# Kernel optimization log

Measured on AMD Instinct MI355X. Metric: run time of the kernel, lower is better.

## Reference

```python
import jax, jax.numpy as jnp
import numpy as np

# ---- config (matches init_kwargs) ----
B, NP, DIM, HEADS, DH, NDIM = 32, 576, 512, 8, 64, 16
N = NP + 1                 # seq len incl cls token = 577
INNER = HEADS * DH         # 512


def setup_inputs() -> dict:
    key = jax.random.key(0)
    ks = jax.random.split(key, 11)
    D2 = 2 * DIM  # bidirectional EMA doubles kernel dim
    return {
        "x": jax.random.normal(ks[0], (B, N, DIM), jnp.float32),
        "W_qk": jax.random.normal(ks[1], (DIM, 2 * INNER), jnp.float32) / np.float32(np.sqrt(DIM)),
        "W_v": jax.random.normal(ks[2], (DIM, INNER), jnp.float32) / np.float32(np.sqrt(DIM)),
        "W_out": jax.random.normal(ks[3], (INNER, DIM), jnp.float32) / np.float32(np.sqrt(INNER)),
        "b_out": jnp.zeros((DIM,), jnp.float32),
        "rel_bias": jax.random.normal(ks[4], (2 * N - 1,), jnp.float32) * 0.02,
        "ema_delta": jax.random.normal(ks[5], (D2, NDIM, 1), jnp.float32),
        "ema_alpha": jax.random.normal(ks[6], (D2, NDIM, 1), jnp.float32),
        "ema_beta": jax.random.normal(ks[7], (D2, NDIM, 1), jnp.float32) * 0.5,
        "ema_gamma": jax.random.normal(ks[8], (D2, NDIM), jnp.float32) * 0.5,
        "ema_omega": jax.random.normal(ks[9], (DIM,), jnp.float32),
    }


def _ema_move(x, delta, alpha, beta, gamma, omega):
    """Bidirectional MultiHeadEMA (MEGA) via FFT convolution. x: (B, L, D)."""
    b, L, d = x.shape
    scale = jnp.asarray(np.sqrt(1.0 / NDIM), x.dtype)
    p = jax.nn.sigmoid(delta)                      # (2D, N, 1)
    q = 1.0 - p * jax.nn.sigmoid(alpha)            # (2D, N, 1), in (0,1)
    vander = jnp.arange(L, dtype=x.dtype)[None, None, :] * jnp.log(q)  # (2D, N, L)
    kern = (p * beta) * jnp.exp(vander)            # (2D, N, L)
    k = jnp.einsum('dnl,dn->dl', kern, gamma * scale)  # (2D, L)
    k1, k2 = k[:d], k[d:]
    # combined bidirectional kernel, length 2L-1
    kk = jnp.pad(k1, ((0, 0), (L - 1, 0))) + jnp.pad(k2[:, ::-1], ((0, 0), (0, L - 1)))
    xt = jnp.pad(x.transpose(0, 2, 1), ((0, 0), (0, 0), (L - 1, 0)))  # (B, D, 2L-1)
    fft_len = 2 * L - 1
    nfft = 2 * fft_len
    out = jnp.fft.irfft(jnp.fft.rfft(xt, n=nfft) * jnp.fft.rfft(kk, n=nfft)[None], n=nfft)
    s = 2 * L - 2
    out = out[..., s:s + L].transpose(0, 2, 1).astype(x.dtype)  # (B, L, D)
    return jax.nn.silu(out + x * omega)


def _rel_pos_bias(rb, seq_len):
    """RelativePositionalBias (MEGA): (2*N-1,) param -> (seq_len, seq_len) bias."""
    max_pos = N
    bvec = rb[max_pos - seq_len: max_pos + seq_len - 1]   # (2*seq_len-1,)
    t = jnp.pad(bvec, (0, seq_len))
    t = jnp.tile(t, seq_len)[:-seq_len].reshape(seq_len, 3 * seq_len - 2)
    r = (2 * seq_len - 1) // 2
    return t[:, r:t.shape[1] - r]


def reference(x, W_qk, W_v, W_out, b_out, rel_bias,
              ema_delta, ema_alpha, ema_beta, ema_gamma, ema_omega):
    b, n, _ = x.shape
    cls_tok = x[:, :1]
    moved = _ema_move(x[:, 1:], ema_delta, ema_alpha, ema_beta, ema_gamma, ema_omega)
    xm = jnp.concatenate([cls_tok, moved], axis=1)        # (B, N, DIM)
    q, k = jnp.split(xm @ W_qk, 2, axis=-1)
    v = xm @ W_v                                          # smooth_v_as_well=True

    def heads(t):
        return t.reshape(b, n, HEADS, DH).transpose(0, 2, 1, 3)  # (B, H, N, DH)

    q, k, v = heads(q), heads(k), heads(v)
    dots = jnp.einsum('bhid,bhjd->bhij', q, k) * (DH ** -0.5)
    attn = jax.nn.softmax(dots, axis=-1)
    attn = attn + _rel_pos_bias(rel_bias, n)[None, None]  # bias added AFTER softmax
    out = jnp.einsum('bhij,bhjd->bhid', attn, v)
    out = out.transpose(0, 2, 1, 3).reshape(b, n, INNER)
    return out @ W_out + b_out
```

## Files before the change

### kernel.cpp

```cpp
#include <hip/hip_runtime.h>

typedef unsigned short ushort;

typedef __bf16 bf16x8 __attribute__((ext_vector_type(8)));
typedef float  f32x4  __attribute__((ext_vector_type(4)));
typedef float  f32x2  __attribute__((ext_vector_type(2)));
typedef unsigned short u16x8 __attribute__((ext_vector_type(8)));
typedef unsigned short u16x4 __attribute__((ext_vector_type(4)));
typedef unsigned int   u32x2 __attribute__((ext_vector_type(2)));

static constexpr int BB   = 32;
static constexpr int NN   = 577;
static constexpr int LL   = 576;
static constexpr int DIMC = 512;
static constexpr int BN   = BB * NN;

static constexpr size_t SZ_WQKVT = 1536ull * 512 * 2;
static constexpr size_t SZ_WOUTT = 512ull * 512 * 2;
static constexpr size_t SZ_QK    = (size_t)BN * 1024 * 2;
static constexpr size_t SZ_V     = (size_t)BN * 512 * 2;
static constexpr size_t SZ_VT    = 256ull * 64 * 640 * 2;
static constexpr size_t OFF_WQKVT = 0;
static constexpr size_t OFF_WOUTT = OFF_WQKVT + SZ_WQKVT;
static constexpr size_t OFF_QTAB  = OFF_WOUTT + SZ_WOUTT;
static constexpr size_t OFF_CTAB  = OFF_QTAB + 65536;
static constexpr size_t OFF_QK    = OFF_CTAB + 65536;
static constexpr size_t OFF_V     = OFF_QK + SZ_QK;
static constexpr size_t OFF_REGION= OFF_V + SZ_V;
static constexpr size_t OFF_XM    = OFF_REGION;
static constexpr size_t OFF_VT    = OFF_REGION;
static constexpr size_t OFF_AO    = OFF_REGION + SZ_VT;
static constexpr size_t OFF_ST    = OFF_AO;
static constexpr size_t WS_NEEDED = OFF_AO + SZ_V;

__device__ __forceinline__ ushort bf16bits(float f) {
  unsigned int u = __builtin_bit_cast(unsigned int, f);
  u = (u + 0x7fffu + ((u >> 16) & 1u)) >> 16;
  return (ushort)u;
}
__device__ __forceinline__ unsigned int bf16pk(float lo, float hi) {
  unsigned int u0 = __builtin_bit_cast(unsigned int, lo);
  unsigned int u1 = __builtin_bit_cast(unsigned int, hi);
  unsigned int a0 = u0 + 0x7fffu + ((u0 >> 16) & 1u);
  unsigned int a1 = u1 + 0x7fffu + ((u1 >> 16) & 1u);
  return __builtin_amdgcn_perm(a1, a0, 0x07060302);
}
__device__ __forceinline__ float sigmoidf_(float z) { return 1.f / (1.f + __expf(-z)); }
__device__ __forceinline__ float siluf(float z)     { return z / (1.f + __expf(-z)); }
__device__ __forceinline__ void gload16(const ushort* g, ushort* l) {
  __builtin_amdgcn_global_load_lds(
      (const __attribute__((address_space(1))) unsigned int*)g,
      (__attribute__((address_space(3))) unsigned int*)l, 16, 0, 0);
}

__global__ __launch_bounds__(256) void k_prep(
    const float* __restrict__ delta, const float* __restrict__ alpha,
    const float* __restrict__ beta,  const float* __restrict__ gamma,
    const float* __restrict__ Wqk,   const float* __restrict__ Wv,
    const float* __restrict__ Wout,
    float* __restrict__ qtab, float* __restrict__ ctab,
    ushort* __restrict__ Wqkvt, ushort* __restrict__ Woutt)
{
  int idx = blockIdx.x * 256 + threadIdx.x;
  if (idx < 16384) {
    float p = sigmoidf_(delta[idx]);
    float q = 1.f - p * sigmoidf_(alpha[idx]);
    qtab[idx] = q;
    ctab[idx] = p * beta[idx] * gamma[idx] * 0.25f;
  }
  int i2 = idx - 16384;
  if (i2 >= 0 && i2 < 1536 * 512) {
    int n = i2 >> 9, k = i2 & 511;
    float w = (n < 1024) ? Wqk[k * 1024 + n] : Wv[k * 512 + (n - 1024)];
    Wqkvt[i2] = bf16bits(w);
  }
  int i3 = i2 - 1536 * 512;
  if (i3 >= 0 && i3 < 512 * 512) {
    int n = i3 >> 9, k = i3 & 511;
    Woutt[i3] = bf16bits(Wout[k * 512 + n]);
  }
}


__global__ __launch_bounds__(64) void k_ema_p1(
    const float* __restrict__ x, const float* __restrict__ qtab,
    float* __restrict__ st)
{
  const int gx = blockIdx.x, cy = blockIdx.y, b = blockIdx.z;
  if (gx < 8) {
    const int d = gx * 64 + threadIdx.x;
    f32x2 q[8], h[8];
    #pragma unroll
    for (int n = 0; n < 8; ++n) {
      q[n] = *(const f32x2*)(qtab + d * 16 + 2 * n);
      h[n] = (f32x2){0.f, 0.f};
    }
    const float* xp = x + ((size_t)b * NN + 1) * DIMC + d;
    const int blo = cy * 9;
    float xn[8];
    #pragma unroll
    for (int u = 0; u < 8; ++u) xn[u] = xp[(blo * 8 + u) * DIMC];
    for (int blk = blo; blk < blo + 9; ++blk) {
      float xv[8];
      #pragma unroll
      for (int u = 0; u < 8; ++u) xv[u] = xn[u];
      if (blk < blo + 8) {
        #pragma unroll
        for (int u = 0; u < 8; ++u) xn[u] = xp[((blk + 1) * 8 + u) * DIMC];
      }
      #pragma unroll
      for (int u = 0; u < 8; ++u) {
        f32x2 x2 = {xv[u], xv[u]};
        #pragma unroll
        for (int n = 0; n < 8; ++n) h[n] = __builtin_elementwise_fma(q[n], h[n], x2);
      }
    }
    float* sp = st + (((size_t)b * 8 + cy) * 16) * 512 + d;
    #pragma unroll
    for (int n = 0; n < 8; ++n) { sp[(2*n) * 512] = h[n][0]; sp[(2*n+1) * 512] = h[n][1]; }
  } else {
    const int d = (gx - 8) * 64 + threadIdx.x;
    f32x2 q[8], g[8];
    #pragma unroll
    for (int n = 0; n < 8; ++n) {
      q[n] = *(const f32x2*)(qtab + (d + 512) * 16 + 2 * n);
      g[n] = (f32x2){0.f, 0.f};
    }
    const float* xp = x + ((size_t)b * NN + 1) * DIMC + d;
    const int blo = (7 - cy) * 9;
    float xn[8];
    #pragma unroll
    for (int u = 0; u < 8; ++u) xn[u] = xp[((blo + 8) * 8 + u) * DIMC];
    for (int blk = blo + 8; blk >= blo; --blk) {
      float xv[8];
      #pragma unroll
      for (int u = 0; u < 8; ++u) xv[u] = xn[u];
      if (blk > blo) {
        #pragma unroll
        for (int u = 0; u < 8; ++u) xn[u] = xp[((blk - 1) * 8 + u) * DIMC];
      }
      #pragma unroll
      for (int u = 7; u >= 0; --u) {
        f32x2 x2 = {xv[u], xv[u]};
        #pragma unroll
        for (int n = 0; n < 8; ++n) g[n] = __builtin_elementwise_fma(q[n], g[n], x2);
      }
    }
    float* sp = st + (((size_t)(32 + b) * 8 + cy) * 16) * 512 + d;
    #pragma unroll
    for (int n = 0; n < 8; ++n) { sp[(2*n) * 512] = g[n][0]; sp[(2*n+1) * 512] = g[n][1]; }
  }
}

__global__ __launch_bounds__(256) void k_ema_mid(
    const float* __restrict__ qtab, float* __restrict__ st)
{
  int idx = blockIdx.x * 256 + threadIdx.x;
  int d = idx & 511;
  int rest = idx >> 9;
  int n = rest & 15;
  int db = rest >> 4;
  int dir = db >> 5;
  float q = qtab[(((size_t)dir << 9) + d) * 16 + n];
  float q2 = q * q, q4 = q2 * q2, q8 = q4 * q4;
  float q16 = q8 * q8, q32 = q16 * q16, q64 = q32 * q32;
  float qL = q64 * q8;
  float h = 0.f;
  float* sp = st + ((size_t)db * 128 + n) * 512 + d;
  #pragma unroll
  for (int c = 0; c < 8; ++c) {
    float tmp = (c < 7) ? sp[c * 8192] : 0.f;
    sp[c * 8192] = h;
    h = fmaf(qL, h, tmp);
  }
}

__global__ __launch_bounds__(64) void k_ema_fuse(
    const float* __restrict__ x, const float* __restrict__ qtab,
    const float* __restrict__ ctab, const float* __restrict__ st,
    const float* __restrict__ omega, ushort* __restrict__ xm)
{
  __shared__ _Float16 yb[72 * 64];
  const int lane = threadIdx.x;
  const int gx = blockIdx.x, cy = blockIdx.y, b = blockIdx.z;
  const int d = gx * 64 + lane;
  const float* xp = x + ((size_t)b * NN + 1 + cy * 72) * DIMC + d;
  {
    f32x2 q[8], c[8], g[8];
    const float* sp = st + (((size_t)(32 + b) * 8 + (7 - cy)) * 16) * 512 + d;
    #pragma unroll
    for (int n = 0; n < 8; ++n) {
      q[n] = *(const f32x2*)(qtab + (d + 512) * 16 + 2 * n);
      c[n] = *(const f32x2*)(ctab + (d + 512) * 16 + 2 * n);
      g[n] = (f32x2){sp[(2*n) * 512], sp[(2*n+1) * 512]};
    }
    float xn[8];
    #pragma unroll
    for (int u = 0; u < 8; ++u) xn[u] = xp[(64 + u) * DIMC];
    for (int blk = 8; blk >= 0; --blk) {
      float xv[8];
      #pragma unroll
      for (int u = 0; u < 8; ++u) xv[u] = xn[u];
      if (blk > 0) {
        #pragma unroll
        for (int u = 0; u < 8; ++u) xn[u] = xp[((blk - 1) * 8 + u) * DIMC];
      }
      #pragma unroll
      for (int u = 7; u >= 0; --u) {
        f32x2 x2 = {xv[u], xv[u]};
        f32x2 yv = {0.f, 0.f};
        #pragma unroll
        for (int n = 0; n < 8; ++n) {
          g[n] = __builtin_elementwise_fma(q[n], g[n], x2);
          yv   = __builtin_elementwise_fma(c[n], g[n], yv);
        }
        yb[(blk * 8 + u) * 64 + lane] = (_Float16)(yv[0] + yv[1]);
      }
    }
  }
  __syncthreads();
  {
    f32x2 q[8], c[8], h[8];
    const float* sp = st + (((size_t)b * 8 + cy) * 16) * 512 + d;
    #pragma unroll
    for (int n = 0; n < 8; ++n) {
      q[n] = *(const f32x2*)(qtab + d * 16 + 2 * n);
      c[n] = *(const f32x2*)(ctab + d * 16 + 2 * n);
      h[n] = (f32x2){sp[(2*n) * 512], sp[(2*n+1) * 512]};
    }
    const float om = omega[d];
    ushort* op = xm + ((size_t)b * NN + 1 + cy * 72) * DIMC + d;
    float xn[8];
    #pragma unroll
    for (int u = 0; u < 8; ++u) xn[u] = xp[u * DIMC];
    for (int blk = 0; blk < 9; ++blk) {
      float xv[8];
      #pragma unroll
      for (int u = 0; u < 8; ++u) xv[u] = xn[u];
      if (blk < 8) {
        #pragma unroll
        for (int u = 0; u < 8; ++u) xn[u] = xp[((blk + 1) * 8 + u) * DIMC];
      }
      #pragma unroll
      for (int u = 0; u < 8; ++u) {
        f32x2 x2 = {xv[u], xv[u]};
        f32x2 yv = {0.f, 0.f};
        #pragma unroll
        for (int n = 0; n < 8; ++n) {
          h[n] = __builtin_elementwise_fma(q[n], h[n], x2);
          yv   = __builtin_elementwise_fma(c[n], h[n], yv);
        }
        float s = (yv[0] + yv[1]) + (float)yb[(blk * 8 + u) * 64 + lane] + xv[u] * om;
        op[(blk * 8 + u) * DIMC] = bf16bits(siluf(s));
      }
    }
  }
  if (cy == 0) {
    size_t e0 = ((size_t)b * NN) * DIMC + d;
    xm[e0] = bf16bits(x[e0]);
  }
}

__global__ __launch_bounds__(256) void k_qkv(
    const ushort* __restrict__ A, const ushort* __restrict__ Bt,
    ushort* __restrict__ qk, ushort* __restrict__ v)
{
  __shared__ alignas(16) ushort lA[128 * 32];
  __shared__ alignas(16) ushort lB[128 * 32];
  const int tid = threadIdx.x, wv = tid >> 6, lane = tid & 63;
  const int quad = lane >> 4, c16 = lane & 15;
  const int fid = blockIdx.y * 12 + blockIdx.x;
  const int xcd = fid & 7, ord = fid >> 3;
  const int wg  = (xcd < 4 ? xcd * 218 : 872 + (xcd - 4) * 217) + ord;
  const int row0 = (wg / 12) * 128, n0 = (wg % 12) * 128;
  const int wm = (wv >> 1) * 64, wn = (wv & 1) * 64;
  const int sr  = wv * 32 + (lane >> 2);
  const int scs = ((lane & 3) ^ (sr & 3)) * 8;
  int ga[2], gb[2];
  #pragma unroll
  for (int s = 0; s < 2; ++s) {
    int r = row0 + sr + s * 16; if (r > BN - 1) r = BN - 1;
    ga[s] = r;
    gb[s] = n0 + sr + s * 16;
  }
  const int xread = (quad ^ (c16 & 3)) * 8;
  f32x4 z4 = {0.f, 0.f, 0.f, 0.f};
  f32x4 acc[4][4];
  #pragma unroll
  for (int mi = 0; mi < 4; ++mi)
    #pragma unroll
    for (int ni = 0; ni < 4; ++ni) acc[mi][ni] = z4;

  for (int kt = 0; kt < 16; ++kt) {
    const int k0 = kt * 32;
    __syncthreads();
    #pragma unroll
    for (int s = 0; s < 2; ++s) {
      gload16(A  + (size_t)ga[s] * 512 + k0 + scs, lA + (wv * 32 + s * 16) * 32);
      gload16(Bt + (size_t)gb[s] * 512 + k0 + scs, lB + (wv * 32 + s * 16) * 32);
    }
    __syncthreads();
    bf16x8 af[4], bfv[4];
    #pragma unroll
    for (int mi = 0; mi < 4; ++mi)
      af[mi] = *(const bf16x8*)(lA + (wm + mi * 16 + c16) * 32 + xread);
    #pragma unroll
    for (int ni = 0; ni < 4; ++ni)
      bfv[ni] = *(const bf16x8*)(lB + (wn + ni * 16 + c16) * 32 + xread);
    #pragma unroll
    for (int mi = 0; mi < 4; ++mi)
      #pragma unroll
      for (int ni = 0; ni < 4; ++ni)
        acc[mi][ni] = __builtin_amdgcn_mfma_f32_16x16x32_bf16(af[mi], bfv[ni], acc[mi][ni], 0, 0, 0);
  }
  const bool isv = (n0 >= 1024);
  const float osc = (n0 < 512) ? 0.1803368801111f : 1.0f;
  #pragma unroll
  for (int mi = 0; mi < 4; ++mi) {
    #pragma unroll
    for (int r = 0; r < 4; ++r) {
      int grow = row0 + wm + mi * 16 + quad * 4 + r;
      if (grow < BN) {
        #pragma unroll
        for (int ni = 0; ni < 4; ++ni) {
          int col = n0 + wn + ni * 16 + c16;
          ushort vb = bf16bits(acc[mi][ni][r] * osc);
          if (!isv) qk[(size_t)grow * 1024 + col] = vb;
          else      v[(size_t)grow * 512 + (col - 1024)] = vb;
        }
      }
    }
  }
}

__global__ __launch_bounds__(256) void k_vtrans(
    const ushort* __restrict__ v, ushort* __restrict__ vt)
{
  __shared__ alignas(16) ushort lt[64 * 72];
  const int tid = threadIdx.x;
  const int bh = blockIdx.y, b = bh >> 3, h = bh & 7;
  const int j0 = blockIdx.x * 64;
  #pragma unroll
  for (int pass = 0; pass < 2; ++pass) {
    int cch = pass * 256 + tid;
    int jl = cch >> 3, cc = cch & 7;
    int gj = j0 + jl;
    u16x8 val = {0, 0, 0, 0, 0, 0, 0, 0};
    if (gj < 577) val = *(const u16x8*)(v + ((size_t)(b * NN + gj)) * 512 + h * 64 + cc * 8);
    *(u16x8*)(lt + jl * 72 + cc * 8) = val;
  }
  __syncthreads();
  #pragma unroll
  for (int pass = 0; pass < 2; ++pass) {
    int cch = pass * 256 + tid;
    int dh = cch >> 3, jc = cch & 7;
    u16x8 o;
    #pragma unroll
    for (int e = 0; e < 8; ++e) o[e] = lt[(jc * 8 + e) * 72 + dh];
    *(u16x8*)(vt + ((size_t)(bh * 64 + dh)) * 640 + j0 + jc * 8) = o;
  }
}

__global__ __launch_bounds__(256) void k_fattn(
    const ushort* __restrict__ qk, const ushort* __restrict__ vt,
    const float* __restrict__ relb, ushort* __restrict__ ao)
{
  __shared__ alignas(16) ushort lk0[64 * 64];
  __shared__ alignas(16) ushort lk1[64 * 64];
  __shared__ alignas(16) ushort lv0[64 * 64];
  __shared__ alignas(16) ushort lv1[64 * 64];
  __shared__ alignas(16) ushort lp[128 * 64];
  __shared__ ushort lbias16[1280];
  const int tid = threadIdx.x, wv = tid >> 6, lane = tid & 63;
  const int quad = lane >> 4, c16 = lane & 15;
  const int bh = blockIdx.x, b = bh >> 3, h = bh & 7;
  const int i0 = blockIdx.y * 128, wm = wv * 32;
  for (int t = tid; t < 1280; t += 256) {
    int idx = t - 64;
    lbias16[t] = (idx >= 0 && idx < 1153) ? bf16bits(relb[idx]) : (ushort)0;
  }
  bf16x8 aq[2][2];
  #pragma unroll
  for (int ms = 0; ms < 2; ++ms) {
    int gi = i0 + wm + ms * 16 + c16; if (gi > 576) gi = 576;
    const ushort* qp = qk + ((size_t)(b * NN + gi)) * 1024 + h * 64;
    #pragma unroll
    for (int kk = 0; kk < 2; ++kk)
      aq[ms][kk] = *(const bf16x8*)(qp + (kk * 4 + quad) * 8);
  }
  const int lr = lane >> 3, lc = lane & 7;
  const ushort* kroot = qk + ((size_t)b * NN) * 1024 + 512 + h * 64;
  const ushort* vroot = vt + ((size_t)bh * 64) * 640;

  float lsum[2] = {0.f, 0.f};
  f32x4 z4 = {0.f, 0.f, 0.f, 0.f};
  f32x4 accp[2][4], accb[2][4];
  #pragma unroll
  for (int ms = 0; ms < 2; ++ms)
    #pragma unroll
    for (int ns = 0; ns < 4; ++ns) { accp[ms][ns] = z4; accb[ms][ns] = z4; }

  #define STAGE_TILE(J0, DK, DV)                                              \
    {                                                                         \
      _Pragma("unroll")                                                       \
      for (int s = 0; s < 2; ++s) {                                           \
        const int r  = wv * 16 + s * 8 + lr;                                  \
        const int sc = (lc ^ (r & 7)) * 8;                                    \
        int gj = (J0) + r; if (gj > 576) gj = 576;                            \
        gload16(kroot + (size_t)gj * 1024 + sc, (DK) + (wv * 16 + s * 8) * 64); \
        gload16(vroot + (size_t)r * 640 + (J0) + sc, (DV) + (wv * 16 + s * 8) * 64); \
      }                                                                       \
    }

  STAGE_TILE(0, lk0, lv0)

  for (int jt = 0; jt < 10; ++jt) {
    const ushort* ck_ = (jt & 1) ? lk1 : lk0;
    const ushort* cv_ = (jt & 1) ? lv1 : lv0;
    ushort* nk_ = (jt & 1) ? lk0 : lk1;
    ushort* nv_ = (jt & 1) ? lv0 : lv1;
    __syncthreads();
    if (jt < 9) STAGE_TILE((jt + 1) * 64, nk_, nv_)
    #pragma unroll
    for (int ms = 0; ms < 2; ++ms) {
      f32x4 dacc[4] = {z4, z4, z4, z4};
      #pragma unroll
      for (int kk = 0; kk < 2; ++kk) {
        const int ck = kk * 4 + quad;
        #pragma unroll
        for (int ns = 0; ns < 4; ++ns) {
          const int row = ns * 16 + c16;
          bf16x8 bk = *(const bf16x8*)(ck_ + row * 64 + ((ck ^ (row & 7)) * 8));
          dacc[ns] = __builtin_amdgcn_mfma_f32_16x16x32_bf16(bk, aq[ms][kk], dacc[ns], 0, 0, 0);
        }
      }
      const int irow = wm + ms * 16 + c16;
      const int xr = irow & 7;
      #pragma unroll
      for (int ns = 0; ns < 4; ++ns) {
        float ex[4];
        #pragma unroll
        for (int r = 0; r < 4; ++r) {
          float e = __builtin_amdgcn_exp2f(dacc[ns][r]);
          if (jt == 9 && (ns * 16 + quad * 4 + r) >= 1) e = 0.f;
          ex[r] = e;
        }
        lsum[ms] += (ex[0] + ex[1]) + (ex[2] + ex[3]);
        u32x2 pw = { bf16pk(ex[0], ex[1]), bf16pk(ex[2], ex[3]) };
        const int lc2 = ns * 2 + (quad >> 1);
        *(u32x2*)(lp + irow * 64 + ((lc2 ^ xr) * 8) + (quad & 1) * 4) = pw;
      }
    }
    const int j0 = jt * 64;
    #pragma unroll
    for (int kk = 0; kk < 2; ++kk) {
      const int ck = kk * 4 + quad;
      bf16x8 ap[2], ab[2];
      #pragma unroll
      for (int ms = 0; ms < 2; ++ms) {
        const int row = wm + ms * 16 + c16;
        ap[ms] = *(const bf16x8*)(lp + row * 64 + ((ck ^ (row & 7)) * 8));
        u16x8 abu;
        const int base = 64 + 576 + j0 + kk * 32 + quad * 8 - (i0 + row);
        #pragma unroll
        for (int e = 0; e < 8; ++e) abu[e] = lbias16[base + e];
        ab[ms] = __builtin_bit_cast(bf16x8, abu);
      }
      #pragma unroll
      for (int ns = 0; ns < 4; ++ns) {
        const int row = ns * 16 + c16;
        bf16x8 bV = *(const bf16x8*)(cv_ + row * 64 + ((ck ^ (row & 7)) * 8));
        #pragma unroll
        for (int ms = 0; ms < 2; ++ms) {
          accp[ms][ns] = __builtin_amdgcn_mfma_f32_16x16x32_bf16(ap[ms], bV, accp[ms][ns], 0, 0, 0);
          accb[ms][ns] = __builtin_amdgcn_mfma_f32_16x16x32_bf16(ab[ms], bV, accb[ms][ns], 0, 0, 0);
        }
      }
    }
  }
  #undef STAGE_TILE
  float tot[2];
  #pragma unroll
  for (int ms = 0; ms < 2; ++ms) {
    float t = lsum[ms];
    t += __shfl_xor(t, 16);
    t += __shfl_xor(t, 32);
    tot[ms] = t;
  }
  #pragma unroll
  for (int ms = 0; ms < 2; ++ms) {
    #pragma unroll
    for (int r = 0; r < 4; ++r) {
      float li = 1.f / __shfl(tot[ms], quad * 4 + r);
      int ii = i0 + wm + ms * 16 + quad * 4 + r;
      if (ii < 577) {
        #pragma unroll
        for (int ns = 0; ns < 4; ++ns)
          ao[((size_t)(b * NN + ii)) * 512 + h * 64 + ns * 16 + c16] =
              bf16bits(accp[ms][ns][r] * li + accb[ms][ns][r]);
      }
    }
  }
}

__global__ __launch_bounds__(256) void k_out(
    const ushort* __restrict__ A, const ushort* __restrict__ Bt,
    const float* __restrict__ bout, float* __restrict__ out)
{
  __shared__ alignas(16) ushort lA[128 * 32];
  __shared__ alignas(16) ushort lB[128 * 32];
  const int tid = threadIdx.x, wv = tid >> 6, lane = tid & 63;
  const int quad = lane >> 4, c16 = lane & 15;
  const int row0 = blockIdx.y * 128, n0 = blockIdx.x * 128;
  const int wm = (wv >> 1) * 64, wn = (wv & 1) * 64;
  const int sr  = wv * 32 + (lane >> 2);
  const int scs = ((lane & 3) ^ (sr & 3)) * 8;
  int ga[2], gb[2];
  #pragma unroll
  for (int s = 0; s < 2; ++s) {
    int r = row0 + sr + s * 16; if (r > BN - 1) r = BN - 1;
    ga[s] = r;
    gb[s] = n0 + sr + s * 16;
  }
  const int xread = (quad ^ (c16 & 3)) * 8;
  f32x4 z4 = {0.f, 0.f, 0.f, 0.f};
  f32x4 acc[4][4];
  #pragma unroll
  for (int mi = 0; mi < 4; ++mi)
    #pragma unroll
    for (int ni = 0; ni < 4; ++ni) acc[mi][ni] = z4;

  for (int kt = 0; kt < 16; ++kt) {
    const int k0 = kt * 32;
    __syncthreads();
    #pragma unroll
    for (int s = 0; s < 2; ++s) {
      gload16(A  + (size_t)ga[s] * 512 + k0 + scs, lA + (wv * 32 + s * 16) * 32);
      gload16(Bt + (size_t)gb[s] * 512 + k0 + scs, lB + (wv * 32 + s * 16) * 32);
    }
    __syncthreads();
    bf16x8 af[4], bfv[4];
    #pragma unroll
    for (int mi = 0; mi < 4; ++mi)
      af[mi] = *(const bf16x8*)(lA + (wm + mi * 16 + c16) * 32 + xread);
    #pragma unroll
    for (int ni = 0; ni < 4; ++ni)
      bfv[ni] = *(const bf16x8*)(lB + (wn + ni * 16 + c16) * 32 + xread);
    #pragma unroll
    for (int mi = 0; mi < 4; ++mi)
      #pragma unroll
      for (int ni = 0; ni < 4; ++ni)
        acc[mi][ni] = __builtin_amdgcn_mfma_f32_16x16x32_bf16(af[mi], bfv[ni], acc[mi][ni], 0, 0, 0);
  }
  #pragma unroll
  for (int mi = 0; mi < 4; ++mi) {
    #pragma unroll
    for (int r = 0; r < 4; ++r) {
      int grow = row0 + wm + mi * 16 + quad * 4 + r;
      if (grow < BN) {
        #pragma unroll
        for (int ni = 0; ni < 4; ++ni) {
          int col = n0 + wn + ni * 16 + c16;
          out[(size_t)grow * 512 + col] = acc[mi][ni][r] + bout[col];
        }
      }
    }
  }
}

extern "C" void kernel_launch(void* const* d_in, const int* in_sizes, int n_in,
                              void* d_out, int out_size, void* d_ws, size_t ws_size,
                              hipStream_t stream) {
  (void)in_sizes; (void)n_in; (void)out_size;
  if (ws_size < WS_NEEDED) return;
  const float* x    = (const float*)d_in[0];
  const float* Wqk  = (const float*)d_in[1];
  const float* Wv   = (const float*)d_in[2];
  const float* Wout = (const float*)d_in[3];
  const float* bout = (const float*)d_in[4];
  const float* relb = (const float*)d_in[5];
  const float* edel = (const float*)d_in[6];
  const float* ealp = (const float*)d_in[7];
  const float* ebet = (const float*)d_in[8];
  const float* egam = (const float*)d_in[9];
  const float* eome = (const float*)d_in[10];

  char* ws = (char*)d_ws;
  ushort* Wqkvt = (ushort*)(ws + OFF_WQKVT);
  ushort* Woutt = (ushort*)(ws + OFF_WOUTT);
  float*  qtab  = (float*)(ws + OFF_QTAB);
  float*  ctab  = (float*)(ws + OFF_CTAB);
  ushort* qkb   = (ushort*)(ws + OFF_QK);
  ushort* vb    = (ushort*)(ws + OFF_V);
  ushort* xm    = (ushort*)(ws + OFF_XM);
  ushort* vtb   = (ushort*)(ws + OFF_VT);
  ushort* aob   = (ushort*)(ws + OFF_AO);
  float*  stf   = (float*)(ws + OFF_ST);
  float*  outp  = (float*)d_out;

  k_prep<<<dim3(4160), dim3(256), 0, stream>>>(edel, ealp, ebet, egam, Wqk, Wv, Wout,
                                               qtab, ctab, Wqkvt, Woutt);
  k_ema_p1<<<dim3(16, 7, 32), dim3(64), 0, stream>>>(x, qtab, stf);
  k_ema_mid<<<dim3(2048), dim3(256), 0, stream>>>(qtab, stf);
  k_ema_fuse<<<dim3(8, 8, 32), dim3(64), 0, stream>>>(x, qtab, ctab, stf, eome, xm);
  k_qkv<<<dim3(12, 145), dim3(256), 0, stream>>>(xm, Wqkvt, qkb, vb);
  k_vtrans<<<dim3(10, 256), dim3(256), 0, stream>>>(vb, vtb);
  k_fattn<<<dim3(256, 5), dim3(256), 0, stream>>>(qkb, vtb, relb, aob);
  k_out<<<dim3(4, 145), dim3(256), 0, stream>>>(aob, Woutt, bout, outp);
}
```

Baseline: 296.9 us.

## Stage QKV GEMM epilogue through LDS and register-prefetch attention K/V tiles

The QKV GEMM epilogue now writes each half of the output tile into shared memory and then emits coalesced 16-byte global stores, replacing scattered 2-byte stores. The attention kernel drops its double-buffered direct global-to-LDS loads. It now prefetches the next K/V tile into registers and writes it into a single LDS buffer after a barrier. This halves K/V LDS usage, which may raise occupancy, at the cost of an extra barrier per tile and more registers.

After: 299.8 us. About the same (+1.0%).

```diff
diff --git a/kernel.cpp b/kernel.cpp
--- a/kernel.cpp
+++ b/kernel.cpp
@@ -265,8 +265,9 @@
     const ushort* __restrict__ A, const ushort* __restrict__ Bt,
     ushort* __restrict__ qk, ushort* __restrict__ v)
 {
-  __shared__ alignas(16) ushort lA[128 * 32];
-  __shared__ alignas(16) ushort lB[128 * 32];
+  __shared__ alignas(16) ushort lsh[8192];
+  ushort* lA = lsh;
+  ushort* lB = lsh + 4096;
   const int tid = threadIdx.x, wv = tid >> 6, lane = tid & 63;
   const int quad = lane >> 4, c16 = lane & 15;
   const int fid = blockIdx.y * 12 + blockIdx.x;
@@ -316,18 +317,29 @@
   const bool isv = (n0 >= 1024);
   const float osc = (n0 < 512) ? 0.1803368801111f : 1.0f;
   #pragma unroll
-  for (int mi = 0; mi < 4; ++mi) {
-    #pragma unroll
-    for (int r = 0; r < 4; ++r) {
-      int grow = row0 + wm + mi * 16 + quad * 4 + r;
+  for (int hh = 0; hh < 2; ++hh) {
+    __syncthreads();
+    if ((wv >> 1) == hh) {
+      #pragma unroll
+      for (int mi = 0; mi < 4; ++mi)
+        #pragma unroll
+        for (int r = 0; r < 4; ++r) {
+          int lrow = mi * 16 + quad * 4 + r;
+          #pragma unroll
+          for (int ni = 0; ni < 4; ++ni)
+            lsh[lrow * 128 + wn + ni * 16 + c16] = bf16bits(acc[mi][ni][r] * osc);
+        }
+    }
+    __syncthreads();
+    #pragma unroll
+    for (int pass = 0; pass < 4; ++pass) {
+      int lrow = pass * 16 + (tid >> 4);
+      int cc = (tid & 15) * 8;
+      int grow = row0 + hh * 64 + lrow;
       if (grow < BN) {
-        #pragma unroll
-        for (int ni = 0; ni < 4; ++ni) {
-          int col = n0 + wn + ni * 16 + c16;
-          ushort vb = bf16bits(acc[mi][ni][r] * osc);
-          if (!isv) qk[(size_t)grow * 1024 + col] = vb;
-          else      v[(size_t)grow * 512 + (col - 1024)] = vb;
-        }
+        u16x8 val = *(const u16x8*)(lsh + lrow * 128 + cc);
+        if (!isv) *(u16x8*)(qk + (size_t)grow * 1024 + n0 + cc) = val;
+        else      *(u16x8*)(v  + (size_t)grow * 512 + (n0 - 1024) + cc) = val;
       }
     }
   }
@@ -365,10 +377,8 @@
     const ushort* __restrict__ qk, const ushort* __restrict__ vt,
     const float* __restrict__ relb, ushort* __restrict__ ao)
 {
-  __shared__ alignas(16) ushort lk0[64 * 64];
-  __shared__ alignas(16) ushort lk1[64 * 64];
-  __shared__ alignas(16) ushort lv0[64 * 64];
-  __shared__ alignas(16) ushort lv1[64 * 64];
+  __shared__ alignas(16) ushort lk[64 * 64];
+  __shared__ alignas(16) ushort lv[64 * 64];
   __shared__ alignas(16) ushort lp[128 * 64];
   __shared__ ushort lbias16[1280];
   const int tid = threadIdx.x, wv = tid >> 6, lane = tid & 63;
@@ -388,9 +398,9 @@
     for (int kk = 0; kk < 2; ++kk)
       aq[ms][kk] = *(const bf16x8*)(qp + (kk * 4 + quad) * 8);
   }
-  const int lr = lane >> 3, lc = lane & 7;
-  const ushort* kroot = qk + ((size_t)b * NN) * 1024 + 512 + h * 64;
-  const ushort* vroot = vt + ((size_t)bh * 64) * 640;
+  const int s_r = tid >> 3, s_c = tid & 7;
+  const ushort* kbase = qk + ((size_t)b * NN) * 1024 + 512 + h * 64 + s_c * 8;
+  const ushort* vbase = vt + ((size_t)bh * 64) * 640 + s_c * 8;
 
   float lsum[2] = {0.f, 0.f};
   f32x4 z4 = {0.f, 0.f, 0.f, 0.f};
@@ -400,27 +410,34 @@
     #pragma unroll
     for (int ns = 0; ns < 4; ++ns) { accp[ms][ns] = z4; accb[ms][ns] = z4; }
 
-  #define STAGE_TILE(J0, DK, DV)                                              \
-    {                                                                         \
-      _Pragma("unroll")                                                       \
-      for (int s = 0; s < 2; ++s) {                                           \
-        const int r  = wv * 16 + s * 8 + lr;                                  \
-        const int sc = (lc ^ (r & 7)) * 8;                                    \
-        int gj = (J0) + r; if (gj > 576) gj = 576;                            \
-        gload16(kroot + (size_t)gj * 1024 + sc, (DK) + (wv * 16 + s * 8) * 64); \
-        gload16(vroot + (size_t)r * 640 + (J0) + sc, (DV) + (wv * 16 + s * 8) * 64); \
-      }                                                                       \
-    }
-
-  STAGE_TILE(0, lk0, lv0)
+  u16x8 sk[2], sv[2];
+  #pragma unroll
+  for (int it = 0; it < 2; ++it) {
+    int r = it * 32 + s_r;
+    sk[it] = *(const u16x8*)(kbase + (size_t)r * 1024);
+    sv[it] = *(const u16x8*)(vbase + (size_t)r * 640);
+  }
 
   for (int jt = 0; jt < 10; ++jt) {
-    const ushort* ck_ = (jt & 1) ? lk1 : lk0;
-    const ushort* cv_ = (jt & 1) ? lv1 : lv0;
-    ushort* nk_ = (jt & 1) ? lk0 : lk1;
-    ushort* nv_ = (jt & 1) ? lv0 : lv1;
-    __syncthreads();
-    if (jt < 9) STAGE_TILE((jt + 1) * 64, nk_, nv_)
+    __syncthreads();
+    #pragma unroll
+    for (int it = 0; it < 2; ++it) {
+      int r = it * 32 + s_r;
+      int pc = (s_c ^ (r & 7)) * 8;
+      *(u16x8*)(lk + r * 64 + pc) = sk[it];
+      *(u16x8*)(lv + r * 64 + pc) = sv[it];
+    }
+    __syncthreads();
+    if (jt < 9) {
+      const int j0n = (jt + 1) * 64;
+      #pragma unroll
+      for (int it = 0; it < 2; ++it) {
+        int r = it * 32 + s_r;
+        int gj = j0n + r; if (gj > 576) gj = 576;
+        sk[it] = *(const u16x8*)(kbase + (size_t)gj * 1024);
+        sv[it] = *(const u16x8*)(vbase + (size_t)r * 640 + j0n);
+      }
+    }
     #pragma unroll
     for (int ms = 0; ms < 2; ++ms) {
       f32x4 dacc[4] = {z4, z4, z4, z4};
@@ -430,7 +447,7 @@
         #pragma unroll
         for (int ns = 0; ns < 4; ++ns) {
           const int row = ns * 16 + c16;
-          bf16x8 bk = *(const bf16x8*)(ck_ + row * 64 + ((ck ^ (row & 7)) * 8));
+          bf16x8 bk = *(const bf16x8*)(lk + row * 64 + ((ck ^ (row & 7)) * 8));
           dacc[ns] = __builtin_amdgcn_mfma_f32_16x16x32_bf16(bk, aq[ms][kk], dacc[ns], 0, 0, 0);
         }
       }
@@ -447,8 +464,8 @@
         }
         lsum[ms] += (ex[0] + ex[1]) + (ex[2] + ex[3]);
         u32x2 pw = { bf16pk(ex[0], ex[1]), bf16pk(ex[2], ex[3]) };
-        const int lc2 = ns * 2 + (quad >> 1);
-        *(u32x2*)(lp + irow * 64 + ((lc2 ^ xr) * 8) + (quad & 1) * 4) = pw;
+        const int lc = ns * 2 + (quad >> 1);
+        *(u32x2*)(lp + irow * 64 + ((lc ^ xr) * 8) + (quad & 1) * 4) = pw;
       }
     }
     const int j0 = jt * 64;
@@ -469,7 +486,7 @@
       #pragma unroll
       for (int ns = 0; ns < 4; ++ns) {
         const int row = ns * 16 + c16;
-        bf16x8 bV = *(const bf16x8*)(cv_ + row * 64 + ((ck ^ (row & 7)) * 8));
+        bf16x8 bV = *(const bf16x8*)(lv + row * 64 + ((ck ^ (row & 7)) * 8));
         #pragma unroll
         for (int ms = 0; ms < 2; ++ms) {
           accp[ms][ns] = __builtin_amdgcn_mfma_f32_16x16x32_bf16(ap[ms], bV, accp[ms][ns], 0, 0, 0);
@@ -478,7 +495,6 @@
       }
     }
   }
-  #undef STAGE_TILE
   float tot[2];
   #pragma unroll
   for (int ms = 0; ms < 2; ++ms) {
```
